# Performance work log

Measured on AMD Instinct MI355X. Metric: run time of the kernel, lower is better.

## Reference

```python
import jax, jax.numpy as jnp
import numpy as np

KSIZE = 3; STRIDE = 1; RATE = 2; FUSE_K = 3; SCALE = 10.0; EPS = 1e-4
B, C, RH, RW = 2, 128, 80, 80  # raw (full-res) feature shape


def setup_inputs() -> dict:
    key = jax.random.key(0)
    ks = jax.random.split(key, 5)
    shp = (B, C, RH, RW)
    names = ["left", "right", "mid", "raw_left", "raw_right"]
    return {n: jax.random.normal(k, shp, dtype=jnp.float32) for n, k in zip(names, ks)}


def _same_pads(H, W, k, s):
    oh, ow = -(-H // s), -(-W // s)
    ph = max(0, (oh - 1) * s + k - H)
    pw = max(0, (ow - 1) * s + k - W)
    return ((ph // 2, ph - ph // 2), (pw // 2, pw - pw // 2))


def extract_patches(x, k, s):
    # torch extract_image_patches with 'same' padding -> (b, L, c, k, k)
    b, c, H, W = x.shape
    pads = _same_pads(H, W, k, s)
    p = jax.lax.conv_general_dilated_patches(x, (k, k), (s, s), pads)  # (b, c*k*k, oh, ow)
    oh, ow = p.shape[2], p.shape[3]
    p = p.reshape(b, c, k, k, oh * ow)  # feature dim is channel-major (c, k, k), like torch unfold
    return p.transpose(0, 4, 1, 2, 3)


def _fuse(s, Hl, Wl, Hm, Wm):
    # diagonal fuse-conv: conv of (b,1,L,P) score image with eye(k), twice with transposes
    b = s.shape[0]
    k = FUSE_K
    eye = jnp.eye(k, dtype=s.dtype).reshape(1, 1, k, k)
    pad = ((k // 2, k // 2), (k // 2, k // 2))
    conv = lambda x: jax.lax.conv_general_dilated(x, eye, (1, 1), pad)
    x = conv(s.reshape(b, 1, Hl * Wl, Hm * Wm))
    x = x.reshape(b, Hl, Wl, Hm, Wm).transpose(0, 2, 1, 4, 3).reshape(b, 1, Wl * Hl, Wm * Hm)
    x = conv(x)
    x = x.reshape(b, Wl, Hl, Wm, Hm).transpose(0, 2, 1, 4, 3)  # (b, Hl, Wl, Hm, Wm)
    return x.reshape(b, Hl * Wl, Hm, Wm)


def _deconv_one(attn, patches):
    # torch conv_transpose2d(attn, patches, stride=RATE, padding=1):
    # conv with lhs dilation RATE, spatially-flipped kernel, padding k-1-1
    kk = patches.shape[-1]
    rhs = jnp.flip(patches, (-2, -1)).transpose(1, 0, 2, 3)  # (C, L, kk, kk)
    p = kk - 1 - 1
    out = jax.lax.conv_general_dilated(attn[None], rhs, (1, 1), ((p, p), (p, p)),
                                       lhs_dilation=(RATE, RATE),
                                       dimension_numbers=('NCHW', 'OIHW', 'NCHW'))
    return out[0]


def _forward(left, right, mid, raw_left, raw_right):
    kernel = 2 * RATE
    rawp_l = extract_patches(raw_left, kernel, RATE * STRIDE)   # (B, L, C, 4, 4)
    rawp_r = extract_patches(raw_right, kernel, RATE * STRIDE)
    # nearest downsample by rate
    l = left[:, :, ::RATE, ::RATE]
    r = right[:, :, ::RATE, ::RATE]
    m = mid[:, :, ::RATE, ::RATE]
    Hl, Wl = l.shape[2], l.shape[3]
    Hm, Wm = m.shape[2], m.shape[3]
    lp = extract_patches(l, KSIZE, STRIDE)   # (B, L, C, 3, 3)
    rp = extract_patches(r, KSIZE, STRIDE)
    mp = extract_patches(m, KSIZE, STRIDE)   # (B, P, C, 3, 3); conv2d(same-padded xi, w) == patch dot

    def norm(p):
        # torch: sqrt(reduce_sum(p^2 + eps)) -- eps added elementwise before the sum
        return p / jnp.sqrt(jnp.sum(p * p + EPS, axis=(2, 3, 4), keepdims=True))

    sl = jnp.einsum('bqcij,bpcij->bqp', norm(lp), mp).reshape(-1, Hl * Wl, Hm, Wm)
    sr = jnp.einsum('bqcij,bpcij->bqp', norm(rp), mp).reshape(-1, Hl * Wl, Hm, Wm)
    sl = _fuse(sl, Hl, Wl, Hm, Wm)
    sr = _fuse(sr, Hl, Wl, Hm, Wm)
    al = jax.nn.softmax(sl * SCALE, axis=1)
    ar = jax.nn.softmax(sr * SCALE, axis=1)
    y_l = jax.vmap(_deconv_one)(al, rawp_l) / 4.0   # (B, C, RH, RW)
    y_r = jax.vmap(_deconv_one)(ar, rawp_r) / 4.0
    # cos_function_weight: cosine blending ramp along width (1 at left edge -> 0 at right edge)
    w = 0.5 * (1.0 + jnp.cos(jnp.pi * jnp.arange(RW, dtype=y_l.dtype) / (RW - 1)))
    w = w.reshape(1, 1, 1, RW)
    return w * y_l + jnp.flip(w, 3) * y_r


def reference(left, right, mid, raw_left, raw_right):
    return _forward(left, right, mid, raw_left, raw_right)
```

## Files before the change

kernel.cpp:

```cpp
#include <hip/hip_runtime.h>
#include <hip/hip_bf16.h>

typedef __hip_bfloat16 bf16;
typedef __attribute__((ext_vector_type(8))) short short8;
typedef __attribute__((ext_vector_type(4))) float f32x4;
typedef unsigned short ushort_t;

#define PI_F 3.14159265358979323846f
#define GPAD_Z 3111696L

#define GLOAD_LDS16(gp, lp)                                                    \
  __builtin_amdgcn_global_load_lds(                                            \
      (const __attribute__((address_space(1))) unsigned int*)(gp),             \
      (__attribute__((address_space(3))) unsigned int*)(lp), 16, 0, 0)

__global__ __launch_bounds__(128) void prep_pt(const float* __restrict__ left,
                                               const float* __restrict__ right,
                                               const float* __restrict__ mid,
                                               bf16* __restrict__ PTe,
                                               bf16* __restrict__ MTe,
                                               float* __restrict__ SQ) {
  int q = blockIdx.x;
  int y = blockIdx.y;
  int c = threadIdx.x;
  int qi = q / 40, qj = q - qi * 40;
  const float* src;
  bf16* dst;
  int b;
  bool aside = (y < 4);
  if (aside) {
    b = y & 1;
    src = (y < 2) ? left : right;
    dst = PTe + (long)y * 1664 * 384;
  } else {
    b = y - 4;
    src = mid;
    dst = MTe + (long)(y - 4) * 1664 * 384;
  }
  float v = src[(((long)b * 128 + c) * 80 + 2 * qi) * 80 + 2 * qj];
  bf16 hi = __float2bfloat16(v);
  bf16 lo = __float2bfloat16(v - __bfloat162float(hi));
  if (aside) {
    dst[(long)q * 384 + c] = hi;
    dst[(long)q * 384 + 128 + c] = lo;
    dst[(long)q * 384 + 256 + c] = hi;
  } else {
    dst[(long)q * 384 + c] = hi;
    dst[(long)q * 384 + 128 + c] = hi;
    dst[(long)q * 384 + 256 + c] = lo;
  }
  if (aside) {
    __shared__ float red[128];
    red[c] = v * v;
    __syncthreads();
    for (int s = 64; s > 0; s >>= 1) {
      if (c < s) red[c] += red[c + s];
      __syncthreads();
    }
    if (c == 0) SQ[y * 1600 + q] = red[0];
  }
}

__global__ void invn_kernel(const float* __restrict__ SQ, float* __restrict__ INV) {
  int idx = blockIdx.x * 256 + threadIdx.x;
  if (idx >= 6400) return;
  int z = idx / 1600, q = idx - z * 1600;
  int qi = q / 40, qj = q - qi * 40;
  float s = 0.1152f;
  #pragma unroll
  for (int di = -1; di <= 1; ++di)
    #pragma unroll
    for (int dj = -1; dj <= 1; ++dj) {
      int a = qi + di, b = qj + dj;
      if (a >= 0 && a < 40 && b >= 0 && b < 40) s += SQ[z * 1600 + a * 40 + b];
    }
  INV[idx] = rsqrtf(s);
}

__global__ __launch_bounds__(256) void padzero_kernel(float* __restrict__ Gp) {
  int row = blockIdx.x;
  int z = blockIdx.y;
  float* R = Gp + (long)z * GPAD_Z + (long)row * 1764;
  int r42 = row % 42;
  if (r42 == 0 || r42 == 41) {
    for (int c = threadIdx.x; c < 1764; c += 256) R[c] = 0.f;
  } else {
    for (int i = threadIdx.x; i < 84; i += 256) {
      int c = (i >> 1) * 42 + ((i & 1) ? 41 : 0);
      R[c] = 0.f;
    }
  }
}

__global__ __launch_bounds__(256) void gemm_nt(const bf16* __restrict__ A,
                                               const bf16* __restrict__ B,
                                               float* __restrict__ C,
                                               int M, int N, int K,
                                               long Az, long Bz, long Cz,
                                               int bmod, int cpad) {
  int z = blockIdx.z;
  A += (long)z * Az;
  B += (long)(bmod ? (z & 1) : z) * Bz;
  C += (long)z * Cz;
  __shared__ bf16 As[128 * 32];
  __shared__ bf16 Bs[128 * 32];
  int lane = threadIdx.x & 63;
  int w = threadIdx.x >> 6;
  int mb = blockIdx.x * 128;
  int nb = blockIdx.y * 128;
  int lr = lane >> 2;
  int gb = (lane & 3) ^ ((lane >> 3) & 3);
  int lm = lane & 15;
  int swz = (lm >> 1) & 3;
  int kb = lane >> 4;
  int pos = (kb ^ swz) * 8;
  int warow = (w >> 1) * 64;
  int wbrow = (w & 1) * 64;
  f32x4 acc[4][4];
  #pragma unroll
  for (int i = 0; i < 4; ++i)
    #pragma unroll
    for (int j = 0; j < 4; ++j) {
      f32x4 zv = {0.f, 0.f, 0.f, 0.f};
      acc[i][j] = zv;
    }
  for (int k0 = 0; k0 < K; k0 += 32) {
    __syncthreads();
    #pragma unroll
    for (int t = 0; t < 2; ++t) {
      int r = (w * 2 + t) * 16 + lr;
      GLOAD_LDS16(A + (long)(mb + r) * K + k0 + gb * 8, As + (w * 2 + t) * 512);
      GLOAD_LDS16(B + (long)(nb + r) * K + k0 + gb * 8, Bs + (w * 2 + t) * 512);
    }
    __syncthreads();
    short8 af[4], bfr[4];
    #pragma unroll
    for (int i = 0; i < 4; ++i) {
      af[i]  = *reinterpret_cast<const short8*>(As + (warow + i * 16 + lm) * 32 + pos);
      bfr[i] = *reinterpret_cast<const short8*>(Bs + (wbrow + i * 16 + lm) * 32 + pos);
    }
    #pragma unroll
    for (int i = 0; i < 4; ++i)
      #pragma unroll
      for (int j = 0; j < 4; ++j)
        acc[i][j] = __builtin_amdgcn_mfma_f32_16x16x32_bf16(af[i], bfr[j], acc[i][j], 0, 0, 0);
  }
  int m0 = mb + warow;
  int n0 = nb + wbrow;
  int col = lane & 15;
  int r0 = (lane >> 4) * 4;
  #pragma unroll
  for (int i = 0; i < 4; ++i)
    #pragma unroll
    for (int j = 0; j < 4; ++j) {
      int n = n0 + j * 16 + col;
      if (n < N) {
        int nc = cpad ? ((n / 40) * 42 + (n - (n / 40) * 40) + 43) : n;
        #pragma unroll
        for (int r = 0; r < 4; ++r) {
          int m = m0 + i * 16 + r0 + r;
          if (m < M) {
            long mr = cpad ? ((long)((m / 40) * 42 + (m - (m / 40) * 40) + 43) * 1764)
                           : ((long)m * N);
            C[mr + nc] = acc[i][j][r];
          }
        }
      }
    }
}

#define BAR() __builtin_amdgcn_s_barrier()
#define LGKM0() asm volatile("s_waitcnt lgkmcnt(0)" ::: "memory")
#define STAGE_A(tt, h)                                                         \
  { long _k = (long)(tt) * 64;                                                 \
    char* _d = lds + (((tt) & 1) << 16) + (((h) * 8 + w) << 11);               \
    GLOAD_LDS16(a_row[h] + _k, _d);                                            \
    GLOAD_LDS16(a_row[h] + _k + 32, _d + 1024); }
#define STAGE_B(tt, h)                                                         \
  { long _k = (long)(tt) * 64;                                                 \
    char* _d = lds + (((tt) & 1) << 16) + 32768 + (((h) * 8 + w) << 11);       \
    GLOAD_LDS16(b_row[h] + _k, _d);                                            \
    GLOAD_LDS16(b_row[h] + _k + 32, _d + 1024); }
#define LD8(off) (*reinterpret_cast<const short8*>(lds + (off)))
#define LOAD_A(bufo, mh)                                                       \
  { _Pragma("unroll") for (int i = 0; i < 4; ++i)                              \
      { _Pragma("unroll") for (int kc = 0; kc < 2; ++kc)                       \
          a[i][kc] = LD8((bufo) + (((wm * 8 + (mh) * 4 + i) * 2 + kc) << 10) + rd_off); } }
#define LOAD_B(dst, bufo, nh)                                                  \
  { _Pragma("unroll") for (int j = 0; j < 2; ++j)                              \
      { _Pragma("unroll") for (int kc = 0; kc < 2; ++kc)                       \
          dst[j][kc] = LD8((bufo) + 32768 + (((wn * 4 + (nh) * 2 + j) * 2 + kc) << 10) + rd_off); } }
#define MFMA16(mh, nh, bset)                                                   \
  { _Pragma("unroll") for (int kc = 0; kc < 2; ++kc)                           \
      { _Pragma("unroll") for (int i = 0; i < 4; ++i)                          \
          { _Pragma("unroll") for (int j = 0; j < 2; ++j)                      \
              acc[(mh) * 4 + i][(nh) * 2 + j] = __builtin_amdgcn_mfma_f32_16x16x32_bf16( \
                  a[i][kc], bset[j][kc], acc[(mh) * 4 + i][(nh) * 2 + j], 0, 0, 0); } } }

__global__ __launch_bounds__(512, 2) void gemm256_nt(const bf16* __restrict__ A,
                                                     const bf16* __restrict__ B,
                                                     float* __restrict__ C,
                                                     int M, int N, int K,
                                                     long Az, long Bz, long Cz,
                                                     int nballoc) {
  __shared__ __align__(16) char lds[131072];
  int z = blockIdx.z;
  A += (long)z * Az;
  B += (long)z * Bz;
  C += (long)z * Cz;
  int tid = threadIdx.x;
  int lane = tid & 63;
  int w = tid >> 6;
  int wm = w >> 2;
  int wn = w & 3;
  int mb = blockIdx.x * 256;
  int nb = blockIdx.y * 256;
  int NT = K >> 6;

  int srcb = (lane << 4) ^ (lane & 32);
  int r_src = srcb >> 6;
  int c_src = (srcb & 63) >> 1;
  const bf16* a_row[2];
  const bf16* b_row[2];
  #pragma unroll
  for (int h = 0; h < 2; ++h) {
    a_row[h] = A + (long)(mb + (h * 8 + w) * 16 + r_src) * K + c_src;
    int br = nb + (h * 8 + w) * 16 + r_src;
    if (br > nballoc - 1) br = nballoc - 1;
    b_row[h] = B + (long)br * K + c_src;
  }
  int rd_off = (((lane & 15) << 6) | ((lane >> 4) << 4)) ^ ((lane & 8) << 2);

  short8 a[4][2], p0[2][2], p1[2][2];
  f32x4 acc[8][4];
  #pragma unroll
  for (int i = 0; i < 8; ++i)
    #pragma unroll
    for (int j = 0; j < 4; ++j) {
      f32x4 zv = {0.f, 0.f, 0.f, 0.f};
      acc[i][j] = zv;
    }

  STAGE_A(0, 0); STAGE_A(0, 1); STAGE_B(0, 0); STAGE_B(0, 1);
  STAGE_A(1, 0); STAGE_A(1, 1); STAGE_B(1, 0);
  asm volatile("s_waitcnt vmcnt(6)" ::: "memory");
  BAR();

  for (int t = 0; t < NT; ++t) {
    int bufo = (t & 1) << 16;
    LOAD_A(bufo, 0);
    LOAD_B(p0, bufo, 0);
    if (t + 1 < NT) STAGE_B(t + 1, 1);
    BAR(); LGKM0();
    __builtin_amdgcn_s_setprio(1); MFMA16(0, 0, p0); __builtin_amdgcn_s_setprio(0);
    BAR();
    LOAD_B(p1, bufo, 1);
    BAR(); LGKM0();
    __builtin_amdgcn_s_setprio(1); MFMA16(0, 1, p1); __builtin_amdgcn_s_setprio(0);
    BAR();
    LOAD_A(bufo, 1);
    BAR(); LGKM0();
    __builtin_amdgcn_s_setprio(1); MFMA16(1, 1, p1); __builtin_amdgcn_s_setprio(0);
    BAR();
    LOAD_B(p0, bufo, 0);
    BAR(); LGKM0();
    __builtin_amdgcn_s_setprio(1); MFMA16(1, 0, p0); __builtin_amdgcn_s_setprio(0);
    BAR();
    if (t + 2 < NT) {
      STAGE_A(t + 2, 0); STAGE_A(t + 2, 1); STAGE_B(t + 2, 0);
      asm volatile("s_waitcnt vmcnt(6)" ::: "memory");
      BAR();
    } else if (t + 1 < NT) {
      asm volatile("s_waitcnt vmcnt(0)" ::: "memory");
      BAR();
    }
  }

  int col = lane & 15;
  int r0 = (lane >> 4) * 4;
  int m_base = mb + wm * 128;
  int n_base = nb + wn * 64;
  #pragma unroll
  for (int i = 0; i < 8; ++i)
    #pragma unroll
    for (int j = 0; j < 4; ++j) {
      int n = n_base + j * 16 + col;
      if (n < N) {
        #pragma unroll
        for (int r = 0; r < 4; ++r) {
          int m = m_base + i * 16 + r0 + r;
          C[(long)m * N + n] = acc[i][j][r];
        }
      }
    }
}

__global__ __launch_bounds__(256) void s1fuse1_kernel(const float* __restrict__ Gp,
                                                      const float* __restrict__ INV,
                                                      float* __restrict__ S2) {
  int p = blockIdx.x * 256 + threadIdx.x;
  if (p >= 1600) return;
  int q = blockIdx.y, z = blockIdx.z;
  const float* Gz = Gp + (long)z * GPAD_Z;
  float s = 0.f;
  #pragma unroll
  for (int d = -1; d <= 1; ++d) {
    int q2 = q + d, p2 = p + d;
    bool ok = ((unsigned)q2 < 1600u) && ((unsigned)p2 < 1600u);
    int q2c = ok ? q2 : 0;
    int p2c = ok ? p2 : 0;
    float wgt = ok ? INV[z * 1600 + q2c] : 0.f;
    int qi = q2c / 40, qj = q2c - qi * 40;
    int pi = p2c / 40, pj = p2c - pi * 40;
    const float* base = Gz + (long)(qi * 42 + qj + 43) * 1764 + (pi * 42 + pj + 43);
    float t = 0.f;
    #pragma unroll
    for (int di = -1; di <= 1; ++di)
      #pragma unroll
      for (int dj = -1; dj <= 1; ++dj)
        t += base[(long)(di * 42 + dj) * 1765];
    s += t * wgt;
  }
  S2[((long)z * 1600 + q) * 1600 + p] = s;
}

__global__ __launch_bounds__(256) void fuse2_kernel(const float* __restrict__ S2,
                                                    float* __restrict__ S3) {
  int p = blockIdx.x * 256 + threadIdx.x;
  if (p >= 1600) return;
  int q = blockIdx.y, z = blockIdx.z;
  const float* S = S2 + (long)z * 2560000;
  int il = q / 40, jl = q - il * 40;
  int im = p / 40, jm = p - im * 40;
  int u = jl * 40 + il, v = jm * 40 + im;
  float s = 0.f;
  #pragma unroll
  for (int d = -1; d <= 1; ++d) {
    int u2 = u + d, v2 = v + d;
    if (u2 >= 0 && u2 < 1600 && v2 >= 0 && v2 < 1600) {
      int q2 = (u2 % 40) * 40 + u2 / 40;
      int p2 = (v2 % 40) * 40 + v2 / 40;
      s += S[(long)q2 * 1600 + p2];
    }
  }
  S3[((long)z * 1600 + q) * 1600 + p] = s;
}

__global__ __launch_bounds__(256) void smax_part(const float* __restrict__ S3,
                                                 float* __restrict__ Pm,
                                                 float* __restrict__ Ps) {
  int z = blockIdx.z, qc = blockIdx.y;
  int pl = threadIdx.x & 63;
  int ql = threadIdx.x >> 6;
  int p = blockIdx.x * 64 + pl;
  const float* S = S3 + (long)z * 2560000;
  float m = -1e30f, s = 0.f;
  for (int i = 0; i < 50; ++i) {
    int q = qc * 200 + i * 4 + ql;
    float x = 10.f * S[(long)q * 1600 + p];
    if (x > m) { s *= __expf(m - x); m = x; }
    s += __expf(x - m);
  }
  __shared__ float lm[4][64], ls[4][64];
  lm[ql][pl] = m;
  ls[ql][pl] = s;
  __syncthreads();
  if (ql == 0) {
    float M = m, SS = s;
    #pragma unroll
    for (int j = 1; j < 4; ++j) {
      float mj = lm[j][pl], sj = ls[j][pl];
      if (mj > M) { SS = SS * __expf(M - mj) + sj; M = mj; }
      else SS += sj * __expf(mj - M);
    }
    Pm[((long)z * 8 + qc) * 1600 + p] = M;
    Ps[((long)z * 8 + qc) * 1600 + p] = SS;
  }
}

__global__ __launch_bounds__(256) void smax_write(const float* __restrict__ S3,
                                                  const float* __restrict__ Pm,
                                                  const float* __restrict__ Ps,
                                                  bf16* __restrict__ AT) {
  int z = blockIdx.z;
  int p0 = blockIdx.x * 64, q0 = blockIdx.y * 64;
  int pl = threadIdx.x & 63, ql = threadIdx.x >> 6;
  __shared__ float lfm[64], lfs[64];
  if (ql == 0) {
    int p = p0 + pl;
    float M = -1e30f;
    #pragma unroll
    for (int c = 0; c < 8; ++c) M = fmaxf(M, Pm[((long)z * 8 + c) * 1600 + p]);
    float S = 0.f;
    #pragma unroll
    for (int c = 0; c < 8; ++c)
      S += Ps[((long)z * 8 + c) * 1600 + p] * __expf(Pm[((long)z * 8 + c) * 1600 + p] - M);
    lfm[pl] = M;
    lfs[pl] = 1.f / S;
  }
  __syncthreads();
  __shared__ ushort_t T[64][66];
  float fm = lfm[pl];
  float fs = lfs[pl];
  const float* S = S3 + (long)z * 2560000;
  #pragma unroll
  for (int i = 0; i < 16; ++i) {
    int qq = ql + i * 4;
    float x = 10.f * S[(long)(q0 + qq) * 1600 + p0 + pl];
    bf16 h = __float2bfloat16(__expf(x - fm) * fs);
    T[pl][qq] = *reinterpret_cast<ushort_t*>(&h);
  }
  __syncthreads();
  int rp = threadIdx.x >> 5;
  int j = threadIdx.x & 31;
  #pragma unroll
  for (int pass = 0; pass < 8; ++pass) {
    int row = pass * 8 + rp;
    unsigned int vv = (unsigned int)T[row][2 * j] | ((unsigned int)T[row][2 * j + 1] << 16);
    *reinterpret_cast<unsigned int*>(AT + ((long)z * 1664 + p0 + row) * 1600 + q0 + 2 * j) = vv;
  }
}

__global__ __launch_bounds__(256) void rawpt_kernel(const float* __restrict__ rawL,
                                                    const float* __restrict__ rawR,
                                                    bf16* __restrict__ RAWPT) {
  int z = blockIdx.z;
  int r = blockIdx.y * 4 + (threadIdx.x >> 6);
  int q = blockIdx.x * 64 + (threadIdx.x & 63);
  const float* raw = ((z < 2) ? rawL : rawR) + (long)(z & 1) * 819200;
  int c = r >> 4, i = (r >> 2) & 3, j = r & 3;
  int qi = q / 40, qj = q - qi * 40;
  int y = 2 * qi + i - 1, x = 2 * qj + j - 1;
  float v = 0.f;
  if (y >= 0 && y < 80 && x >= 0 && x < 80) v = raw[((long)c * 80 + y) * 80 + x];
  RAWPT[((long)z * 2048 + r) * 1600 + q] = __float2bfloat16(v);
}

__global__ __launch_bounds__(256) void paste_kernel(const float* __restrict__ Z,
                                                    float* __restrict__ out) {
  int idx = blockIdx.x * 256 + threadIdx.x;
  int x = idx % 80;
  int t = idx / 80;
  int y = t % 80;
  t /= 80;
  int c = t % 128;
  int b = t / 128;
  int imA = (y - 1) >> 1, ipA = y - 2 * imA + 1;
  int jmA = (x - 1) >> 1, jpA = x - 2 * jmA + 1;
  const long zs = 2048L * 1600;
  const float* ZL = Z + (long)b * zs;
  const float* ZR = Z + (long)(2 + b) * zs;
  float aL = 0.f, aR = 0.f;
  #pragma unroll
  for (int a = 0; a < 2; ++a) {
    int im = imA + a, ip = ipA - 2 * a;
    if (im < 0 || im > 39) continue;
    #pragma unroll
    for (int e = 0; e < 2; ++e) {
      int jm = jmA + e, jp = jpA - 2 * e;
      if (jm < 0 || jm > 39) continue;
      long off = (long)((c << 4) + ip * 4 + jp) * 1600 + im * 40 + jm;
      aL += ZL[off];
      aR += ZR[off];
    }
  }
  float wx = 0.5f * (1.f + cosf(PI_F * x / 79.f));
  float wf = 0.5f * (1.f + cosf(PI_F * (79 - x) / 79.f));
  out[idx] = 0.25f * (wx * aL + wf * aR);
}

extern "C" void kernel_launch(void* const* d_in, const int* in_sizes, int n_in,
                              void* d_out, int out_size, void* d_ws, size_t ws_size,
                              hipStream_t stream) {
  const float* left  = (const float*)d_in[0];
  const float* right = (const float*)d_in[1];
  const float* mid   = (const float*)d_in[2];
  const float* rawL  = (const float*)d_in[3];
  const float* rawR  = (const float*)d_in[4];
  float* out = (float*)d_out;
  char* ws = (char*)d_ws;

  bf16*  PTe   = (bf16*)(ws + 0);
  bf16*  MTe   = (bf16*)(ws + 5111808);
  float* SQ    = (float*)(ws + 7667712);
  float* INV   = (float*)(ws + 7693312);
  float* Pm    = (float*)(ws + 7718912);
  float* Ps    = (float*)(ws + 7923712);
  float* X     = (float*)(ws + 8179712);
  float* Y     = (float*)(ws + 60608512);
  bf16*  AT    = (bf16*)(ws + 101568512);
  bf16*  RAWPT = (bf16*)Y;

  prep_pt<<<dim3(1600, 6, 1), 128, 0, stream>>>(left, right, mid, PTe, MTe, SQ);
  invn_kernel<<<25, 256, 0, stream>>>(SQ, INV);
  padzero_kernel<<<dim3(1764, 4), 256, 0, stream>>>(X);
  gemm_nt<<<dim3(13, 13, 4), 256, 0, stream>>>(PTe, MTe, X, 1600, 1600, 384,
                                               1664L * 384, 1664L * 384, GPAD_Z, 1, 1);
  s1fuse1_kernel<<<dim3(7, 1600, 4), 256, 0, stream>>>(X, INV, Y);
  fuse2_kernel<<<dim3(7, 1600, 4), 256, 0, stream>>>(Y, X);
  smax_part<<<dim3(25, 8, 4), 256, 0, stream>>>(X, Pm, Ps);
  smax_write<<<dim3(25, 25, 4), 256, 0, stream>>>(X, Pm, Ps, AT);
  rawpt_kernel<<<dim3(25, 512, 4), 256, 0, stream>>>(rawL, rawR, RAWPT);
  gemm256_nt<<<dim3(8, 7, 4), 512, 0, stream>>>(RAWPT, AT, X, 2048, 1600, 1600,
                                                2048L * 1600, 1664L * 1600, 2048L * 1600, 1664);
  paste_kernel<<<6400, 256, 0, stream>>>(X, out);
}
```

Before: 340.3 us.

## Vectorize fuse kernels to 4 outputs per thread with shared column sums

After: 313.9 us. 1.08x faster.

```diff
diff --git a/kernel.cpp b/kernel.cpp
--- a/kernel.cpp
+++ b/kernel.cpp
@@ -4,6 +4,7 @@
 typedef __hip_bfloat16 bf16;
 typedef __attribute__((ext_vector_type(8))) short short8;
 typedef __attribute__((ext_vector_type(4))) float f32x4;
+typedef float f32x4u __attribute__((ext_vector_type(4), aligned(4)));
 typedef unsigned short ushort_t;
 
 #define PI_F 3.14159265358979323846f
@@ -295,55 +296,115 @@
     }
 }
 
+__device__ __forceinline__ float ps9(const float* __restrict__ Gz, int q2, int p2) {
+  int qi2 = q2 / 40, qj2 = q2 - qi2 * 40;
+  int pi2 = p2 / 40, pj2 = p2 - pi2 * 40;
+  const float* base = Gz + (long)(qi2 * 42 + qj2 + 43) * 1764 + (pi2 * 42 + pj2 + 43);
+  float t = 0.f;
+  #pragma unroll
+  for (int di = -1; di <= 1; ++di)
+    #pragma unroll
+    for (int dj = -1; dj <= 1; ++dj)
+      t += base[(long)(di * 42 + dj) * 1765];
+  return t;
+}
+
 __global__ __launch_bounds__(256) void s1fuse1_kernel(const float* __restrict__ Gp,
                                                       const float* __restrict__ INV,
                                                       float* __restrict__ S2) {
-  int p = blockIdx.x * 256 + threadIdx.x;
-  if (p >= 1600) return;
-  int q = blockIdx.y, z = blockIdx.z;
+  int z = blockIdx.y;
+  int bx = blockIdx.x;
+  int xc = bx & 7, rest = bx >> 3;
+  int lid = (xc < 4 ? xc * 313 : 1252 + (xc - 4) * 312) + rest;
+  unsigned int gid = (unsigned int)lid * 256u + threadIdx.x;
+  int q = gid / 400u;
+  int quad = gid - q * 400u;
+  int p0 = quad * 4;
+  int qi = q / 40, qj = q - qi * 40;
+  int pi = p0 / 40, pj0 = p0 - pi * 40;
   const float* Gz = Gp + (long)z * GPAD_Z;
-  float s = 0.f;
-  #pragma unroll
-  for (int d = -1; d <= 1; ++d) {
-    int q2 = q + d, p2 = p + d;
-    bool ok = ((unsigned)q2 < 1600u) && ((unsigned)p2 < 1600u);
-    int q2c = ok ? q2 : 0;
-    int p2c = ok ? p2 : 0;
-    float wgt = ok ? INV[z * 1600 + q2c] : 0.f;
-    int qi = q2c / 40, qj = q2c - qi * 40;
-    int pi = p2c / 40, pj = p2c - pi * 40;
-    const float* base = Gz + (long)(qi * 42 + qj + 43) * 1764 + (pi * 42 + pj + 43);
-    float t = 0.f;
-    #pragma unroll
-    for (int di = -1; di <= 1; ++di)
+  const float* IVz = INV + z * 1600;
+  float* Srow = S2 + ((long)z * 1600 + q) * 1600 + p0;
+
+  if (qj >= 1 && qj <= 38) {
+    long R0C0 = (long)(qi * 42 + qj + 43) * 1764 + (pi * 42 + pj0 + 43);
+    f32x4 cs[5];
+    #pragma unroll
+    for (int s = 0; s < 5; ++s) {
+      const float* pb = Gz + R0C0 + (long)(s - 2) * 1765;
+      f32x4 a0 = *(const f32x4u*)(pb - 42 * 1765);
+      f32x4 a1 = *(const f32x4u*)(pb);
+      f32x4 a2 = *(const f32x4u*)(pb + 42 * 1765);
+      cs[s] = a0 + a1 + a2;
+    }
+    f32x4 c12 = cs[1] + cs[2];
+    f32x4 c23 = cs[2] + cs[3];
+    f32x4 psm = cs[0] + c12;
+    f32x4 ps0 = c12 + cs[3];
+    f32x4 psp = c23 + cs[4];
+    if (pj0 == 0) {
+      int p2 = p0 - 1;
+      psm[0] = (p2 >= 0) ? ps9(Gz, q - 1, p2) : 0.f;
+    } else if (pj0 == 36) {
+      int p2 = p0 + 4;
+      psp[3] = (p2 < 1600) ? ps9(Gz, q + 1, p2) : 0.f;
+    }
+    float wm = IVz[q - 1], w0 = IVz[q], wp = IVz[q + 1];
+    f32x4 outv = psm * wm + ps0 * w0 + psp * wp;
+    *reinterpret_cast<f32x4*>(Srow) = outv;
+  } else {
+    f32x4 outv;
+    #pragma unroll
+    for (int t = 0; t < 4; ++t) {
+      int p = p0 + t;
+      float s = 0.f;
       #pragma unroll
-      for (int dj = -1; dj <= 1; ++dj)
-        t += base[(long)(di * 42 + dj) * 1765];
-    s += t * wgt;
-  }
-  S2[((long)z * 1600 + q) * 1600 + p] = s;
+      for (int d = -1; d <= 1; ++d) {
+        int q2 = q + d, p2 = p + d;
+        bool ok = ((unsigned)q2 < 1600u) && ((unsigned)p2 < 1600u);
+        if (ok) s += IVz[q2] * ps9(Gz, q2, p2);
+      }
+      outv[t] = s;
+    }
+    *reinterpret_cast<f32x4*>(Srow) = outv;
+  }
 }
 
 __global__ __launch_bounds__(256) void fuse2_kernel(const float* __restrict__ S2,
                                                     float* __restrict__ S3) {
-  int p = blockIdx.x * 256 + threadIdx.x;
-  if (p >= 1600) return;
-  int q = blockIdx.y, z = blockIdx.z;
+  int z = blockIdx.y;
+  int bx = blockIdx.x;
+  int xc = bx & 7, rest = bx >> 3;
+  int lid = (xc < 4 ? xc * 313 : 1252 + (xc - 4) * 312) + rest;
+  unsigned int gid = (unsigned int)lid * 256u + threadIdx.x;
+  int q = gid / 400u;
+  int quad = gid - q * 400u;
+  int p0 = quad * 4;
   const float* S = S2 + (long)z * 2560000;
   int il = q / 40, jl = q - il * 40;
-  int im = p / 40, jm = p - im * 40;
-  int u = jl * 40 + il, v = jm * 40 + im;
-  float s = 0.f;
+  int im = p0 / 40, jm = p0 - im * 40;
+  int u = jl * 40 + il;
+  f32x4 acc = {0.f, 0.f, 0.f, 0.f};
   #pragma unroll
   for (int d = -1; d <= 1; ++d) {
-    int u2 = u + d, v2 = v + d;
-    if (u2 >= 0 && u2 < 1600 && v2 >= 0 && v2 < 1600) {
-      int q2 = (u2 % 40) * 40 + u2 / 40;
-      int p2 = (v2 % 40) * 40 + v2 / 40;
-      s += S[(long)q2 * 1600 + p2];
-    }
-  }
-  S3[((long)z * 1600 + q) * 1600 + p] = s;
+    int u2 = u + d;
+    if ((unsigned)u2 >= 1600u) continue;
+    int q2 = (u2 % 40) * 40 + u2 / 40;
+    int imd = im + d;
+    if ((unsigned)imd < 40u) {
+      acc += *reinterpret_cast<const f32x4*>(S + (long)q2 * 1600 + imd * 40 + jm);
+    } else {
+      #pragma unroll
+      for (int t = 0; t < 4; ++t) {
+        int v2 = (jm + t) * 40 + im + d;
+        if ((unsigned)v2 < 1600u) {
+          int p2 = (v2 % 40) * 40 + v2 / 40;
+          acc[t] += S[(long)q2 * 1600 + p2];
+        }
+      }
+    }
+  }
+  *reinterpret_cast<f32x4*>(S3 + ((long)z * 1600 + q) * 1600 + p0) = acc;
 }
 
 __global__ __launch_bounds__(256) void smax_part(const float* __restrict__ S3,
@@ -496,8 +557,8 @@
   padzero_kernel<<<dim3(1764, 4), 256, 0, stream>>>(X);
   gemm_nt<<<dim3(13, 13, 4), 256, 0, stream>>>(PTe, MTe, X, 1600, 1600, 384,
                                                1664L * 384, 1664L * 384, GPAD_Z, 1, 1);
-  s1fuse1_kernel<<<dim3(7, 1600, 4), 256, 0, stream>>>(X, INV, Y);
-  fuse2_kernel<<<dim3(7, 1600, 4), 256, 0, stream>>>(Y, X);
+  s1fuse1_kernel<<<dim3(2500, 4), 256, 0, stream>>>(X, INV, Y);
+  fuse2_kernel<<<dim3(2500, 4), 256, 0, stream>>>(Y, X);
   smax_part<<<dim3(25, 8, 4), 256, 0, stream>>>(X, Pm, Ps);
   smax_write<<<dim3(25, 25, 4), 256, 0, stream>>>(X, Pm, Ps, AT);
   rawpt_kernel<<<dim3(25, 512, 4), 256, 0, stream>>>(rawL, rawR, RAWPT);
```
